# Kernel optimization log

Measured on AMD Instinct MI355X. Metric: run time of the kernel, lower is better.

Reference implementation:

```python
import jax, jax.numpy as jnp
import numpy as np

H = 50  # hidden size fixed by the module


def setup_inputs() -> dict:
    key = jax.random.key(0)
    ks = jax.random.split(key, 7)
    B, T = 2048, 512
    s = 1.0 / np.sqrt(H)  # PyTorch default uniform(-1/sqrt(H), 1/sqrt(H)) scale, approximated with scaled normals
    return {
        "x": jax.random.normal(ks[0], (B, T, 1), dtype=jnp.float32),
        "W_ih": jax.random.normal(ks[1], (4 * H, 1), dtype=jnp.float32) * s,
        "W_hh": jax.random.normal(ks[2], (4 * H, H), dtype=jnp.float32) * s,
        "b_ih": jax.random.normal(ks[3], (4 * H,), dtype=jnp.float32) * s,
        "b_hh": jax.random.normal(ks[4], (4 * H,), dtype=jnp.float32) * s,
        "W_lin": jax.random.normal(ks[5], (1, H), dtype=jnp.float32) * s,
        "b_lin": jax.random.normal(ks[6], (1,), dtype=jnp.float32) * s,
    }


def reference(x, W_ih, W_hh, b_ih, b_hh, W_lin, b_lin):
    B, T, _ = x.shape
    # Precompute input projection for all timesteps: [B, T, 4H]
    xproj = jnp.einsum('bti,gi->btg', x, W_ih) + b_ih + b_hh
    xproj_t = jnp.transpose(xproj, (1, 0, 2))  # [T, B, 4H] for scan over time

    h0 = jnp.zeros((B, H), dtype=x.dtype)
    c0 = jnp.zeros((B, H), dtype=x.dtype)

    def step(carry, xt):
        h, c = carry
        gates = xt + h @ W_hh.T  # [B, 4H]
        i, f, g, o = jnp.split(gates, 4, axis=-1)  # PyTorch gate order i,f,g,o
        i = jax.nn.sigmoid(i)
        f = jax.nn.sigmoid(f)
        g = jnp.tanh(g)
        o = jax.nn.sigmoid(o)
        c = f * c + i * g
        h = o * jnp.tanh(c)
        return (h, c), None

    (h_last, _), _ = jax.lax.scan(step, (h0, c0), xproj_t)
    # x[:, -1, :] of LSTM output == final hidden state h_T
    return h_last @ W_lin.T + b_lin  # [B, 1]
```

## Files before the change

kernel.cpp:

```cpp
#include <hip/hip_runtime.h>

#define HSZ 50
#define TSZ 512
#define NB  8
#define KPAD 72

typedef _Float16 half8  __attribute__((ext_vector_type(8)));
typedef _Float16 half2v __attribute__((ext_vector_type(2)));
typedef float   floatx4 __attribute__((ext_vector_type(4)));

__device__ __forceinline__ float sig_y(float y) {
    return __builtin_amdgcn_rcpf(1.0f + __builtin_amdgcn_exp2f(y));
}
__device__ __forceinline__ float tanh_y(float y) {
    return fmaf(-2.0f, __builtin_amdgcn_rcpf(1.0f + __builtin_amdgcn_exp2f(y)), 1.0f);
}

__global__ __launch_bounds__(256)
void lstm_mir(const float* __restrict__ x,
              const float* __restrict__ W_ih,
              const float* __restrict__ W_hh,
              const float* __restrict__ b_ih,
              const float* __restrict__ b_hh,
              const float* __restrict__ W_lin,
              const float* __restrict__ b_lin,
              float* __restrict__ out)
{
    __shared__ float xs[TSZ][NB];
    __shared__ __align__(16) _Float16 hlds[2][16][KPAD];

    const int tid = threadIdx.x;
    const int w   = tid >> 6;
    const int ln  = tid & 63;
    const int n   = ln & 15;
    const int q   = ln >> 4;
    const int hi  = (n >> 3) & 1;
    const int nb  = n & 7;
    const int b0  = blockIdx.x * NB;

    const float* xg = x + (size_t)b0 * TSZ;
    for (int i = tid; i < NB * TSZ; i += 256)
        xs[i & (TSZ - 1)][i >> 9] = xg[i];
    for (int i = tid; i < 2 * 16 * KPAD; i += 256)
        ((_Float16*)hlds)[i] = (i % KPAD == 50) ? (_Float16)1.0f : (_Float16)0.0f;

    const int uA = 16 * w + n;
    half8 af[4][2];
#pragma unroll
    for (int g = 0; g < 4; ++g) {
        const float gs = (g == 2) ? 2.88539008f : -1.44269504f;
        const int row = g * HSZ + uA;
        const bool rok = (uA < HSZ);
#pragma unroll
        for (int kt = 0; kt < 2; ++kt) {
#pragma unroll
            for (int j = 0; j < 8; ++j) {
                const int k = kt * 32 + q * 8 + j;
                float v = 0.0f;
                if (rok) {
                    if (k < HSZ)      v = W_hh[row * HSZ + k];
                    else if (k == 50) v = b_ih[row] + b_hh[row];
                    else if (k == 51) v = W_ih[row];
                }
                af[g][kt][j] = (_Float16)(v * gs);
            }
        }
    }

    float c0 = 0.0f, c1 = 0.0f;
    __syncthreads();
    if (tid < 16)
        hlds[0][tid][51] = (_Float16)xs[0][tid & 7];
    __syncthreads();

    const floatx4 zero4 = {0.0f, 0.0f, 0.0f, 0.0f};
    const int kcol = 16 * w + 4 * q + 2 * hi;
    _Float16* const hwp0 = &hlds[0][nb][kcol];
    _Float16* const hwp1 = &hlds[1][nb][kcol];
    const bool xlane = (w == 3) && (q == 0) && (hi == 1);

#pragma unroll 2
    for (int t = 0; t < TSZ; ++t) {
        const int rb = t & 1, wb = rb ^ 1;

        const half8 bf0 = *(const half8*)&hlds[rb][n][q * 8];
        const half8 bf1 = *(const half8*)&hlds[rb][n][32 + q * 8];

        float xnext = 0.0f;
        if (w == 3) xnext = xs[(t + 1) & (TSZ - 1)][ln & 7];

        floatx4 acc[4];
#pragma unroll
        for (int g = 0; g < 4; ++g) {
            acc[g] = __builtin_amdgcn_mfma_f32_16x16x32_f16(af[g][0], bf0, zero4,  0, 0, 0);
            acc[g] = __builtin_amdgcn_mfma_f32_16x16x32_f16(af[g][1], bf1, acc[g], 0, 0, 0);
        }

        float pa[4], pb[4];
#pragma unroll
        for (int g = 0; g < 4; ++g) {
            pa[g] = hi ? acc[g][2] : acc[g][0];
            pb[g] = hi ? acc[g][3] : acc[g][1];
        }

        const float i0 = sig_y (pa[0]);
        const float f0 = sig_y (pa[1]);
        const float g0 = tanh_y(pa[2]);
        const float o0 = sig_y (pa[3]);
        const float i1 = sig_y (pb[0]);
        const float f1 = sig_y (pb[1]);
        const float g1 = tanh_y(pb[2]);
        const float o1 = sig_y (pb[3]);
        c0 = fmaf(f0, c0, i0 * g0);
        c1 = fmaf(f1, c1, i1 * g1);
        float h0 = o0 * tanh_y(c0 * 2.88539008f);
        float h1 = o1 * tanh_y(c1 * 2.88539008f);
        if (xlane) { h0 = 1.0f; h1 = xnext; }

        _Float16* const hw = wb ? hwp1 : hwp0;
        const half2v hv = {(_Float16)h0, (_Float16)h1};
        *(half2v*)hw = hv;
        *(half2v*)(hw + 8 * KPAD) = hv;
        __syncthreads();
    }

    if (w == 0 && ln < NB) {
        float acc = b_lin[0];
        for (int u = 0; u < HSZ; ++u)
            acc = fmaf((float)hlds[0][ln][u], W_lin[u], acc);
        out[(size_t)b0 + ln] = acc;
    }
}

extern "C" void kernel_launch(void* const* d_in, const int* in_sizes, int n_in,
                              void* d_out, int out_size, void* d_ws, size_t ws_size,
                              hipStream_t stream) {
    const float* x     = (const float*)d_in[0];
    const float* W_ih  = (const float*)d_in[1];
    const float* W_hh  = (const float*)d_in[2];
    const float* b_ih  = (const float*)d_in[3];
    const float* b_hh  = (const float*)d_in[4];
    const float* W_lin = (const float*)d_in[5];
    const float* b_lin = (const float*)d_in[6];
    float* outp = (float*)d_out;

    const int B = in_sizes[0] / TSZ;
    hipLaunchKernelGGL(lstm_mir, dim3(B / NB), dim3(256), 0, stream,
                       x, W_ih, W_hh, b_ih, b_hh, W_lin, b_lin, outp);
}
```

Measured before the change: 244.7 us.

## Halve batch per block so each lane computes one hidden unit per step

Cuts the batch rows per workgroup from 8 to 4. Each lane now handles one (unit, batch) pair instead of two, and each row of the 16-wide MFMA B tile is replicated four times. Grid size doubles to 512 blocks, which spreads the serial recurrence across more CUs and halves the per-lane transcendental work on the critical path of each time step. The cost is redundant MFMA work per useful batch row, four scalar LDS stores per step instead of two vector stores, and more blocks contending for CUs.

```diff
diff --git a/kernel.cpp b/kernel.cpp
--- a/kernel.cpp
+++ b/kernel.cpp
@@ -2,11 +2,10 @@
 
 #define HSZ 50
 #define TSZ 512
-#define NB  8
+#define NB  4
 #define KPAD 72
 
 typedef _Float16 half8  __attribute__((ext_vector_type(8)));
-typedef _Float16 half2v __attribute__((ext_vector_type(2)));
 typedef float   floatx4 __attribute__((ext_vector_type(4)));
 
 __device__ __forceinline__ float sig_y(float y) {
@@ -17,14 +16,14 @@
 }
 
 __global__ __launch_bounds__(256)
-void lstm_mir(const float* __restrict__ x,
-              const float* __restrict__ W_ih,
-              const float* __restrict__ W_hh,
-              const float* __restrict__ b_ih,
-              const float* __restrict__ b_hh,
-              const float* __restrict__ W_lin,
-              const float* __restrict__ b_lin,
-              float* __restrict__ out)
+void lstm_mir4(const float* __restrict__ x,
+               const float* __restrict__ W_ih,
+               const float* __restrict__ W_hh,
+               const float* __restrict__ b_ih,
+               const float* __restrict__ b_hh,
+               const float* __restrict__ W_lin,
+               const float* __restrict__ b_lin,
+               float* __restrict__ out)
 {
     __shared__ float xs[TSZ][NB];
     __shared__ __align__(16) _Float16 hlds[2][16][KPAD];
@@ -34,8 +33,8 @@
     const int ln  = tid & 63;
     const int n   = ln & 15;
     const int q   = ln >> 4;
-    const int hi  = (n >> 3) & 1;
-    const int nb  = n & 7;
+    const int rr  = n >> 2;
+    const int bb  = n & 3;
     const int b0  = blockIdx.x * NB;
 
     const float* xg = x + (size_t)b0 * TSZ;
@@ -67,17 +66,18 @@
         }
     }
 
-    float c0 = 0.0f, c1 = 0.0f;
+    float c0 = 0.0f;
     __syncthreads();
     if (tid < 16)
-        hlds[0][tid][51] = (_Float16)xs[0][tid & 7];
+        hlds[0][tid][51] = (_Float16)xs[0][tid & 3];
     __syncthreads();
 
     const floatx4 zero4 = {0.0f, 0.0f, 0.0f, 0.0f};
-    const int kcol = 16 * w + 4 * q + 2 * hi;
-    _Float16* const hwp0 = &hlds[0][nb][kcol];
-    _Float16* const hwp1 = &hlds[1][nb][kcol];
-    const bool xlane = (w == 3) && (q == 0) && (hi == 1);
+    const int u = 16 * w + 4 * q + rr;
+    _Float16* const hwp0 = &hlds[0][bb][u];
+    _Float16* const hwp1 = &hlds[1][bb][u];
+    const bool xl50 = (w == 3) && (q == 0) && (rr == 2);
+    const bool xl51 = (w == 3) && (q == 0) && (rr == 3);
 
 #pragma unroll 2
     for (int t = 0; t < TSZ; ++t) {
@@ -87,7 +87,7 @@
         const half8 bf1 = *(const half8*)&hlds[rb][n][32 + q * 8];
 
         float xnext = 0.0f;
-        if (w == 3) xnext = xs[(t + 1) & (TSZ - 1)][ln & 7];
+        if (w == 3) xnext = xs[(t + 1) & (TSZ - 1)][ln & 3];
 
         floatx4 acc[4];
 #pragma unroll
@@ -96,38 +96,36 @@
             acc[g] = __builtin_amdgcn_mfma_f32_16x16x32_f16(af[g][1], bf1, acc[g], 0, 0, 0);
         }
 
-        float pa[4], pb[4];
+        float pre[4];
 #pragma unroll
         for (int g = 0; g < 4; ++g) {
-            pa[g] = hi ? acc[g][2] : acc[g][0];
-            pb[g] = hi ? acc[g][3] : acc[g][1];
+            const float v01 = (rr & 1) ? acc[g][1] : acc[g][0];
+            const float v23 = (rr & 1) ? acc[g][3] : acc[g][2];
+            pre[g] = (rr & 2) ? v23 : v01;
         }
 
-        const float i0 = sig_y (pa[0]);
-        const float f0 = sig_y (pa[1]);
-        const float g0 = tanh_y(pa[2]);
-        const float o0 = sig_y (pa[3]);
-        const float i1 = sig_y (pb[0]);
-        const float f1 = sig_y (pb[1]);
-        const float g1 = tanh_y(pb[2]);
-        const float o1 = sig_y (pb[3]);
+        const float i0 = sig_y (pre[0]);
+        const float f0 = sig_y (pre[1]);
+        const float g0 = tanh_y(pre[2]);
+        const float o0 = sig_y (pre[3]);
         c0 = fmaf(f0, c0, i0 * g0);
-        c1 = fmaf(f1, c1, i1 * g1);
         float h0 = o0 * tanh_y(c0 * 2.88539008f);
-        float h1 = o1 * tanh_y(c1 * 2.88539008f);
-        if (xlane) { h0 = 1.0f; h1 = xnext; }
+        if (xl50) h0 = 1.0f;
+        if (xl51) h0 = xnext;
 
+        const _Float16 hh = (_Float16)h0;
         _Float16* const hw = wb ? hwp1 : hwp0;
-        const half2v hv = {(_Float16)h0, (_Float16)h1};
-        *(half2v*)hw = hv;
-        *(half2v*)(hw + 8 * KPAD) = hv;
+        hw[0]         = hh;
+        hw[4  * KPAD] = hh;
+        hw[8  * KPAD] = hh;
+        hw[12 * KPAD] = hh;
         __syncthreads();
     }
 
     if (w == 0 && ln < NB) {
         float acc = b_lin[0];
-        for (int u = 0; u < HSZ; ++u)
-            acc = fmaf((float)hlds[0][ln][u], W_lin[u], acc);
+        for (int uu = 0; uu < HSZ; ++uu)
+            acc = fmaf((float)hlds[0][ln][uu], W_lin[uu], acc);
         out[(size_t)b0 + ln] = acc;
     }
 }
@@ -145,6 +143,6 @@
     float* outp = (float*)d_out;
 
     const int B = in_sizes[0] / TSZ;
-    hipLaunchKernelGGL(lstm_mir, dim3(B / NB), dim3(256), 0, stream,
+    hipLaunchKernelGGL(lstm_mir4, dim3(B / NB), dim3(256), 0, stream,
                        x, W_ih, W_hh, b_ih, b_hh, W_lin, b_lin, outp);
 }
```

After: 262.3 us. +7.2%, slower.
